# Optimization experiments

Measured on AMD Instinct MI355X. Metric: run time of the kernel, lower is better.

## Reference

```python
import jax, jax.numpy as jnp
import numpy as np

B, T, F, H = 16, 1024, 1024, 16
D = F // H  # 64

def setup_inputs() -> dict:
    key = jax.random.key(0)
    k0, k1, k2 = jax.random.split(key, 3)
    return {
        "x": jax.random.normal(k0, (B, T, F), jnp.float32),
        "mask": jnp.zeros((B, 1, T, 1), jnp.float32),
        "W_attn": jax.random.normal(k1, (F, 3 * F), jnp.float32) * 0.02,
        "b_attn": jnp.zeros((3 * F,), jnp.float32),
        "W_proj": jax.random.normal(k2, (F, F), jnp.float32) * 0.02,
        "b_proj": jnp.zeros((F,), jnp.float32),
    }

def reference(x, mask, W_attn, b_attn, W_proj, b_proj):
    # qkv projection (Conv1D == linear with transposed weight layout)
    qkv = x @ W_attn + b_attn                       # [B,T,3F]
    q, k, v = jnp.split(qkv, 3, axis=-1)
    split = lambda t: t.reshape(B, T, H, D).transpose(0, 2, 1, 3)  # [B,H,T,D]
    q, k, v = split(q), split(k), split(v)
    # non-standard: contract over T -> [B,H,D,D] score matrix
    s = jnp.einsum('bhtd,bhte->bhde', q, k) / jnp.sqrt(jnp.float32(D))
    tril = jnp.tril(jnp.ones((D, D), bool))         # bias buffer sliced to DxD
    s = jnp.where(tril, s, jnp.float32(-10000.0))
    # second matmul with V (before softmax), scaled by dk^2
    w = jnp.einsum('bhde,bhte->bhtd', s, v) / (jnp.float32(D) ** 2)  # [B,H,T,D]
    w = jax.nn.softmax(w + mask, axis=-2)           # softmax over T (dim=-2)
    a = w * v                                        # elementwise, not weighted sum
    merge = lambda t: t.transpose(0, 2, 1, 3).reshape(B, T, F)
    a = merge(a) @ W_proj + b_proj                   # output projection
    return a, merge(w)
```

## Files before the change

### kernel.cpp

```cpp
#include <hip/hip_runtime.h>
#include <math.h>

namespace {
constexpr int B = 16, T = 1024, F = 1024, H = 16, D = 64;
constexpr int NT = B * T;
constexpr int QKV_COLS = 3 * F;

constexpr size_t XHI_OFF = 0;
constexpr size_t XLO_OFF = 33554432;
constexpr size_t WAH_OFF = 67108864;
constexpr size_t WVL_OFF = 73400320;
constexpr size_t QB_OFF  = 75497472;
constexpr size_t KB_OFF  = 109051904;
constexpr size_t SB_OFF  = 142606336;
constexpr size_t AB_OFF  = 146800640;
constexpr size_t WPB_OFF = 180355072;
constexpr size_t VB_OFF   = QB_OFF;
constexpr size_t WRAW_OFF = XHI_OFF;
constexpr size_t SP_OFF   = WVL_OFF;
}

typedef __attribute__((ext_vector_type(8))) __bf16 bf16x8;
typedef __attribute__((ext_vector_type(4))) float f32x4;

__device__ __forceinline__ unsigned short f2bf(float f) {
  unsigned u = __builtin_bit_cast(unsigned, f);
  u += 0x7FFFu + ((u >> 16) & 1u);
  return (unsigned short)(u >> 16);
}
__device__ __forceinline__ float bf2f(unsigned short s) {
  return __builtin_bit_cast(float, (unsigned)s << 16);
}
__device__ __forceinline__ void gld16(const unsigned short* g, unsigned short* l) {
  __builtin_amdgcn_global_load_lds(
      (const __attribute__((address_space(1))) unsigned int*)g,
      (__attribute__((address_space(3))) unsigned int*)l, 16, 0, 0);
}

__global__ __launch_bounds__(256) void cast_x(const float* __restrict__ x,
                                              unsigned short* __restrict__ xhi,
                                              unsigned short* __restrict__ xlo) {
  int i = (blockIdx.x * 256 + threadIdx.x) * 4;
  float4 v = *(const float4*)&x[i];
  ushort4 h, l;
  h.x = f2bf(v.x); l.x = f2bf(v.x - bf2f(h.x));
  h.y = f2bf(v.y); l.y = f2bf(v.y - bf2f(h.y));
  h.z = f2bf(v.z); l.z = f2bf(v.z - bf2f(h.z));
  h.w = f2bf(v.w); l.w = f2bf(v.w - bf2f(h.w));
  *(ushort4*)&xhi[i] = h;
  *(ushort4*)&xlo[i] = l;
}

__global__ __launch_bounds__(256) void tcast(const float* __restrict__ W,
                                             unsigned short* __restrict__ Wt,
                                             unsigned short* __restrict__ Wlo,
                                             int ncols, int locol0) {
  __shared__ float tile[64][65];
  const int bx = blockIdx.x, by = blockIdx.y, tid = threadIdx.x;
#pragma unroll
  for (int i = 0; i < 16; ++i) {
    int idx = tid + i * 256;
    int r = idx >> 6, c = idx & 63;
    tile[r][c] = W[(size_t)(by * 64 + r) * ncols + bx * 64 + c];
  }
  __syncthreads();
#pragma unroll
  for (int i = 0; i < 16; ++i) {
    int idx = tid + i * 256;
    int r = idx >> 6, c = idx & 63;
    int col = bx * 64 + r;
    float w = tile[c][r];
    unsigned short h = f2bf(w);
    Wt[(size_t)col * 1024 + by * 64 + c] = h;
    if (col >= locol0) {
      Wlo[(size_t)(col - locol0) * 1024 + by * 64 + c] = f2bf(w - bf2f(h));
    }
  }
}

__device__ __forceinline__ void stage256(const unsigned short* __restrict__ Ag,
                                         const unsigned short* __restrict__ Bg,
                                         int row0, int col0, int kin,
                                         unsigned short* lbase, int wave,
                                         int lane) {
  const int rsub = lane >> 3;
  const int logb = ((lane & 7) ^ rsub) << 4;
  const int isB = logb >> 6;
  const int koff = kin + ((logb & 63) >> 1);
#pragma unroll
  for (int L = 0; L < 4; ++L) {
    const int R0 = (L * 8 + wave) * 8;
    const int r = R0 + rsub;
    const unsigned short* src =
        isB ? (Bg + (size_t)(col0 + r) * 1024 + koff)
            : (Ag + (size_t)(row0 + r) * 1024 + koff);
    gld16(src, lbase + (size_t)R0 * 64);
  }
}

template <int MODE>
__global__ __launch_bounds__(512, 2) void gemm256(
    const unsigned short* __restrict__ A0, const unsigned short* __restrict__ A1,
    const unsigned short* __restrict__ B0, const unsigned short* __restrict__ B1,
    const float* __restrict__ bias, void* __restrict__ out0,
    void* __restrict__ out1) {
  __shared__ __align__(16) unsigned short lds[2][256][64];
  const int tid = threadIdx.x;
  const int wave = tid >> 6, lane = tid & 63;
  const int wr = wave >> 2, wc = wave & 3;
  const int m16 = lane & 15, quad = lane >> 4;
  const int row0 = blockIdx.y * 256, col0 = blockIdx.x * 256;
  constexpr int NKT = (MODE == 1) ? 96 : 32;
  f32x4 acc[8][4] = {};

  stage256(A0, B0, row0, col0, 0, &lds[0][0][0], wave, lane);

  int cur = 0;
  for (int kt = 0; kt < NKT; ++kt) {
    if (kt + 1 < NKT) {
      const unsigned short* Ag = A0;
      const unsigned short* Bg = B0;
      int kin;
      if constexpr (MODE == 1) {
        const int kn = kt + 1, seg = kn >> 5;
        kin = (kn & 31) << 5;
        if (seg == 1) Ag = A1;
        if (seg == 2) Bg = B1;
      } else {
        kin = (kt + 1) << 5;
      }
      stage256(Ag, Bg, row0, col0, kin, &lds[cur ^ 1][0][0], wave, lane);
      asm volatile("s_waitcnt vmcnt(4)" ::: "memory");
    } else {
      asm volatile("s_waitcnt vmcnt(0)" ::: "memory");
    }
    __builtin_amdgcn_s_barrier();

    const char* tb = (const char*)&lds[cur][0][0];
#pragma unroll
    for (int ph = 0; ph < 2; ++ph) {
      bf16x8 af[4], bfr[4];
#pragma unroll
      for (int i = 0; i < 4; ++i) {
        const int r = wr * 128 + (ph * 4 + i) * 16 + m16;
        af[i] = *(const bf16x8*)(tb + r * 128 +
                                 ((quad * 16) ^ ((r & 7) << 4)));
      }
#pragma unroll
      for (int j = 0; j < 4; ++j) {
        const int c = wc * 64 + j * 16 + m16;
        bfr[j] = *(const bf16x8*)(tb + c * 128 +
                                  ((64 + quad * 16) ^ ((c & 7) << 4)));
      }
      __builtin_amdgcn_s_barrier();
      asm volatile("s_waitcnt lgkmcnt(0)" ::: "memory");
      __builtin_amdgcn_sched_barrier(0);
      __builtin_amdgcn_s_setprio(1);
#pragma unroll
      for (int i = 0; i < 4; ++i)
#pragma unroll
        for (int j = 0; j < 4; ++j)
          acc[ph * 4 + i][j] = __builtin_amdgcn_mfma_f32_16x16x32_bf16(
              af[i], bfr[j], acc[ph * 4 + i][j], 0, 0, 0);
      __builtin_amdgcn_s_setprio(0);
      __builtin_amdgcn_s_barrier();
    }
    cur ^= 1;
  }

  if constexpr (MODE == 0) {
    unsigned short* dst = (col0 >= 1024) ? (unsigned short*)out1
                                         : (unsigned short*)out0;
#pragma unroll
    for (int j = 0; j < 4; ++j) {
      const int gcol = col0 + wc * 64 + j * 16 + m16;
      const int f = gcol & 1023;
      const int h = f >> 6, dd = f & 63;
      const float bv = bias[gcol];
#pragma unroll
      for (int i = 0; i < 8; ++i) {
#pragma unroll
        for (int r = 0; r < 4; ++r) {
          const int grow = row0 + wr * 128 + i * 16 + quad * 4 + r;
          const int b = grow >> 10, t = grow & 1023;
          dst[(((size_t)b * H + h) * T + t) * D + dd] = f2bf(acc[i][j][r] + bv);
        }
      }
    }
  } else if constexpr (MODE == 1) {
    float* vbp = (float*)out0;
#pragma unroll
    for (int j = 0; j < 4; ++j) {
      const int f = col0 + wc * 64 + j * 16 + m16;
      const int h = f >> 6, dd = f & 63;
      const float bv = bias[f];
#pragma unroll
      for (int i = 0; i < 8; ++i) {
#pragma unroll
        for (int r = 0; r < 4; ++r) {
          const int grow = row0 + wr * 128 + i * 16 + quad * 4 + r;
          const int b = grow >> 10, t = grow & 1023;
          vbp[(((size_t)b * H + h) * T + t) * D + dd] = acc[i][j][r] + bv;
        }
      }
    }
  } else {
    float* o = (float*)out0;
#pragma unroll
    for (int j = 0; j < 4; ++j) {
      const int gcol = col0 + wc * 64 + j * 16 + m16;
      const float bv = bias[gcol];
#pragma unroll
      for (int i = 0; i < 8; ++i) {
#pragma unroll
        for (int r = 0; r < 4; ++r) {
          const int grow = row0 + wr * 128 + i * 16 + quad * 4 + r;
          o[(size_t)grow * F + gcol] = acc[i][j][r] + bv;
        }
      }
    }
  }
}

__global__ __launch_bounds__(256) void score_kernel(
    const unsigned short* __restrict__ qb, const unsigned short* __restrict__ kb,
    float* __restrict__ sb) {
  __shared__ float qs[64][65];
  __shared__ float ks[64][65];
  const int bh = blockIdx.x;
  const int tid = threadIdx.x;
  const size_t base = (size_t)bh * T * D;
  const int d0 = (tid >> 4) * 4, e0 = (tid & 15) * 4;
  float acc[4][4] = {};
  for (int ch = 0; ch < T / 64; ++ch) {
#pragma unroll
    for (int i = 0; i < 4; ++i) {
      int idx = (tid + i * 256) * 4;
      ushort4 qv = *(const ushort4*)&qb[base + (size_t)ch * 4096 + idx];
      ushort4 kv = *(const ushort4*)&kb[base + (size_t)ch * 4096 + idx];
      int r = idx >> 6, c = idx & 63;
      qs[r][c] = bf2f(qv.x); qs[r][c+1] = bf2f(qv.y);
      qs[r][c+2] = bf2f(qv.z); qs[r][c+3] = bf2f(qv.w);
      ks[r][c] = bf2f(kv.x); ks[r][c+1] = bf2f(kv.y);
      ks[r][c+2] = bf2f(kv.z); ks[r][c+3] = bf2f(kv.w);
    }
    __syncthreads();
#pragma unroll 8
    for (int tt = 0; tt < 64; ++tt) {
      float qa[4], kv[4];
#pragma unroll
      for (int i = 0; i < 4; ++i) qa[i] = qs[tt][d0 + i];
#pragma unroll
      for (int j = 0; j < 4; ++j) kv[j] = ks[tt][e0 + j];
#pragma unroll
      for (int i = 0; i < 4; ++i)
#pragma unroll
        for (int j = 0; j < 4; ++j) acc[i][j] += qa[i] * kv[j];
    }
    __syncthreads();
  }
#pragma unroll
  for (int i = 0; i < 4; ++i) {
#pragma unroll
    for (int j = 0; j < 4; ++j) {
      int dd = d0 + i, ee = e0 + j;
      float v = acc[i][j] * 0.125f;
      if (ee > dd) v = -10000.0f;
      sb[(size_t)bh * (D * D) + dd * D + ee] = v;
    }
  }
}

__global__ __launch_bounds__(256) void exp_kernel(
    const float* __restrict__ vb, const float* __restrict__ sb,
    const float* __restrict__ mask, float* __restrict__ wraw,
    float* __restrict__ sp) {
  const int tc = blockIdx.x, bh = blockIdx.y;
  const int b = bh >> 4;
  const int tid = threadIdx.x;
  const int lane = tid & 63;
  const int dg = __builtin_amdgcn_readfirstlane(tid >> 6);
  const int tg = tc * 64 + lane;
  const float* vrow = vb + (size_t)bh * (T * D) + (size_t)tg * D;
  float4 vreg[16];
#pragma unroll
  for (int i = 0; i < 16; ++i) vreg[i] = *(const float4*)&vrow[i * 4];
  const float mval = mask[(size_t)b * T + tg];
  float ex[16];
#pragma unroll
  for (int dd = 0; dd < 16; ++dd) {
    const int d = dg * 16 + dd;
    const float* srow = sb + (size_t)bh * 4096 + (size_t)d * 64;
    float acc = 0.f;
#pragma unroll
    for (int e4 = 0; e4 < 16; ++e4) {
      float4 s4 = *(const float4*)&srow[e4 * 4];
      acc += s4.x * vreg[e4].x + s4.y * vreg[e4].y +
             s4.z * vreg[e4].z + s4.w * vreg[e4].w;
    }
    float w = acc * (1.0f / 4096.0f) + mval;
    ex[dd] = __expf(w);
    wraw[(size_t)bh * (T * D) + (size_t)d * T + tg] = ex[dd];
  }
#pragma unroll
  for (int dd = 0; dd < 16; ++dd) {
    float v = ex[dd];
    v += __shfl_xor(v, 1, 64);
    v += __shfl_xor(v, 2, 64);
    v += __shfl_xor(v, 4, 64);
    v += __shfl_xor(v, 8, 64);
    v += __shfl_xor(v, 16, 64);
    v += __shfl_xor(v, 32, 64);
    if (lane == 0) sp[((size_t)bh * 16 + tc) * 64 + dg * 16 + dd] = v;
  }
}

__global__ __launch_bounds__(256) void norm_kernel(
    const float* __restrict__ vb, const float* __restrict__ wraw,
    const float* __restrict__ sp, unsigned short* __restrict__ ab,
    float* __restrict__ out2) {
  __shared__ float wt[64][65];
  __shared__ float invS[64];
  const int tc = blockIdx.x, bh = blockIdx.y;
  const int b = bh >> 4, h = bh & 15;
  const int tid = threadIdx.x;
  if (tid < 64) {
    float S = 0.f;
#pragma unroll
    for (int j = 0; j < 16; ++j) S += sp[((size_t)bh * 16 + j) * 64 + tid];
    invS[tid] = 1.0f / S;
  }
#pragma unroll
  for (int i = 0; i < 16; ++i) {
    int idx = tid + i * 256;
    int dd = idx >> 6, tt = idx & 63;
    wt[dd][tt] = wraw[(size_t)bh * (T * D) + (size_t)dd * T + tc * 64 + tt];
  }
  __syncthreads();
  const int d = tid & 63, trow = tid >> 6;
#pragma unroll
  for (int j = 0; j < 16; ++j) {
    int tl = trow * 16 + j;
    int tg = tc * 64 + tl;
    float o = wt[d][tl] * invS[d];
    float vv = vb[(size_t)bh * (T * D) + (size_t)tg * D + d];
    size_t oidx = ((size_t)b * T + tg) * F + h * 64 + d;
    out2[oidx] = o;
    ab[oidx] = f2bf(o * vv);
  }
}

extern "C" void kernel_launch(void* const* d_in, const int* in_sizes, int n_in,
                              void* d_out, int out_size, void* d_ws,
                              size_t ws_size, hipStream_t stream) {
  const float* x = (const float*)d_in[0];
  const float* mask = (const float*)d_in[1];
  const float* Wa = (const float*)d_in[2];
  const float* ba = (const float*)d_in[3];
  const float* Wp = (const float*)d_in[4];
  const float* bp = (const float*)d_in[5];
  char* ws = (char*)d_ws;
  float* out = (float*)d_out;

  unsigned short* xhi = (unsigned short*)(ws + XHI_OFF);
  unsigned short* xlo = (unsigned short*)(ws + XLO_OFF);
  unsigned short* Wah = (unsigned short*)(ws + WAH_OFF);
  unsigned short* Wvl = (unsigned short*)(ws + WVL_OFF);
  unsigned short* qb  = (unsigned short*)(ws + QB_OFF);
  unsigned short* kb  = (unsigned short*)(ws + KB_OFF);
  float* sb   = (float*)(ws + SB_OFF);
  unsigned short* ab  = (unsigned short*)(ws + AB_OFF);
  unsigned short* Wpb = (unsigned short*)(ws + WPB_OFF);
  float* vb   = (float*)(ws + VB_OFF);
  float* wraw = (float*)(ws + WRAW_OFF);
  float* sp   = (float*)(ws + SP_OFF);

  cast_x<<<NT * F / 1024, 256, 0, stream>>>(x, xhi, xlo);
  tcast<<<dim3(QKV_COLS / 64, F / 64), 256, 0, stream>>>(Wa, Wah, Wvl,
                                                         QKV_COLS, 2048);
  tcast<<<dim3(F / 64, F / 64), 256, 0, stream>>>(Wp, Wpb, Wvl, F, 1 << 30);

  gemm256<0><<<dim3(2048 / 256, NT / 256), 512, 0, stream>>>(
      xhi, nullptr, Wah, nullptr, ba, qb, kb);

  score_kernel<<<dim3(B * H), 256, 0, stream>>>(qb, kb, sb);

  gemm256<1><<<dim3(F / 256, NT / 256), 512, 0, stream>>>(
      xhi, xlo, Wah + (size_t)2048 * 1024, Wvl, ba + 2048, vb, nullptr);

  exp_kernel<<<dim3(T / 64, B * H), 256, 0, stream>>>(vb, sb, mask, wraw, sp);

  norm_kernel<<<dim3(T / 64, B * H), 256, 0, stream>>>(
      vb, wraw, sp, ab, out + (size_t)NT * F);

  gemm256<2><<<dim3(F / 256, NT / 256), 512, 0, stream>>>(
      ab, nullptr, Wpb, nullptr, bp, out, nullptr);
}
```

Baseline: 638.4 us.

## Deepen GEMM LDS pipeline to four buffers with three tiles in flight

New measurement: 630.3 us. Within noise of the previous version (-1.3%).

```diff
diff --git a/kernel.cpp b/kernel.cpp
--- a/kernel.cpp
+++ b/kernel.cpp
@@ -99,12 +99,29 @@
 }
 
 template <int MODE>
+__device__ __forceinline__ void tile_src(
+    int kt, const unsigned short* __restrict__ A0,
+    const unsigned short* __restrict__ A1,
+    const unsigned short* __restrict__ B0,
+    const unsigned short* __restrict__ B1,
+    const unsigned short*& Ag, const unsigned short*& Bg, int& kin) {
+  if constexpr (MODE == 1) {
+    const int seg = kt >> 5;
+    kin = (kt & 31) << 5;
+    Ag = (seg == 1) ? A1 : A0;
+    Bg = (seg == 2) ? B1 : B0;
+  } else {
+    Ag = A0; Bg = B0; kin = kt << 5;
+  }
+}
+
+template <int MODE>
 __global__ __launch_bounds__(512, 2) void gemm256(
     const unsigned short* __restrict__ A0, const unsigned short* __restrict__ A1,
     const unsigned short* __restrict__ B0, const unsigned short* __restrict__ B1,
     const float* __restrict__ bias, void* __restrict__ out0,
     void* __restrict__ out1) {
-  __shared__ __align__(16) unsigned short lds[2][256][64];
+  __shared__ __align__(16) unsigned short lds[4][256][64];
   const int tid = threadIdx.x;
   const int wave = tid >> 6, lane = tid & 63;
   const int wr = wave >> 2, wc = wave & 3;
@@ -113,59 +130,64 @@
   constexpr int NKT = (MODE == 1) ? 96 : 32;
   f32x4 acc[8][4] = {};
 
-  stage256(A0, B0, row0, col0, 0, &lds[0][0][0], wave, lane);
-
-  int cur = 0;
+#pragma unroll
+  for (int p = 0; p < 3; ++p) {
+    const unsigned short *Ag, *Bg; int kin;
+    tile_src<MODE>(p, A0, A1, B0, B1, Ag, Bg, kin);
+    stage256(Ag, Bg, row0, col0, kin, &lds[p][0][0], wave, lane);
+  }
+
   for (int kt = 0; kt < NKT; ++kt) {
-    if (kt + 1 < NKT) {
-      const unsigned short* Ag = A0;
-      const unsigned short* Bg = B0;
-      int kin;
-      if constexpr (MODE == 1) {
-        const int kn = kt + 1, seg = kn >> 5;
-        kin = (kn & 31) << 5;
-        if (seg == 1) Ag = A1;
-        if (seg == 2) Bg = B1;
-      } else {
-        kin = (kt + 1) << 5;
-      }
-      stage256(Ag, Bg, row0, col0, kin, &lds[cur ^ 1][0][0], wave, lane);
-      asm volatile("s_waitcnt vmcnt(4)" ::: "memory");
+    if (kt + 3 < NKT) {
+      const unsigned short *Ag, *Bg; int kin;
+      tile_src<MODE>(kt + 3, A0, A1, B0, B1, Ag, Bg, kin);
+      stage256(Ag, Bg, row0, col0, kin, &lds[(kt + 3) & 3][0][0], wave, lane);
+      asm volatile("s_waitcnt vmcnt(12)" ::: "memory");
     } else {
-      asm volatile("s_waitcnt vmcnt(0)" ::: "memory");
+      const int rem = NKT - 1 - kt;
+      if (rem == 2)      asm volatile("s_waitcnt vmcnt(8)" ::: "memory");
+      else if (rem == 1) asm volatile("s_waitcnt vmcnt(4)" ::: "memory");
+      else               asm volatile("s_waitcnt vmcnt(0)" ::: "memory");
     }
     __builtin_amdgcn_s_barrier();
-
-    const char* tb = (const char*)&lds[cur][0][0];
-#pragma unroll
-    for (int ph = 0; ph < 2; ++ph) {
-      bf16x8 af[4], bfr[4];
-#pragma unroll
-      for (int i = 0; i < 4; ++i) {
-        const int r = wr * 128 + (ph * 4 + i) * 16 + m16;
-        af[i] = *(const bf16x8*)(tb + r * 128 +
-                                 ((quad * 16) ^ ((r & 7) << 4)));
-      }
-#pragma unroll
-      for (int j = 0; j < 4; ++j) {
-        const int c = wc * 64 + j * 16 + m16;
-        bfr[j] = *(const bf16x8*)(tb + c * 128 +
-                                  ((64 + quad * 16) ^ ((c & 7) << 4)));
-      }
-      __builtin_amdgcn_s_barrier();
-      asm volatile("s_waitcnt lgkmcnt(0)" ::: "memory");
-      __builtin_amdgcn_sched_barrier(0);
-      __builtin_amdgcn_s_setprio(1);
-#pragma unroll
-      for (int i = 0; i < 4; ++i)
-#pragma unroll
-        for (int j = 0; j < 4; ++j)
-          acc[ph * 4 + i][j] = __builtin_amdgcn_mfma_f32_16x16x32_bf16(
-              af[i], bfr[j], acc[ph * 4 + i][j], 0, 0, 0);
-      __builtin_amdgcn_s_setprio(0);
-      __builtin_amdgcn_s_barrier();
-    }
-    cur ^= 1;
+    __builtin_amdgcn_sched_barrier(0);
+
+    const char* tb = (const char*)&lds[kt & 3][0][0];
+    bf16x8 bfr[4], af0[4], af1[4];
+#pragma unroll
+    for (int j = 0; j < 4; ++j) {
+      const int c = wc * 64 + j * 16 + m16;
+      bfr[j] = *(const bf16x8*)(tb + c * 128 +
+                                ((64 + quad * 16) ^ ((c & 7) << 4)));
+    }
+#pragma unroll
+    for (int i = 0; i < 4; ++i) {
+      const int r = wr * 128 + i * 16 + m16;
+      af0[i] = *(const bf16x8*)(tb + r * 128 +
+                                ((quad * 16) ^ ((r & 7) << 4)));
+    }
+#pragma unroll
+    for (int i = 0; i < 4; ++i) {
+      const int r = wr * 128 + 64 + i * 16 + m16;
+      af1[i] = *(const bf16x8*)(tb + r * 128 +
+                                ((quad * 16) ^ ((r & 7) << 4)));
+    }
+    __builtin_amdgcn_s_setprio(1);
+#pragma unroll
+    for (int i = 0; i < 4; ++i)
+#pragma unroll
+      for (int j = 0; j < 4; ++j)
+        acc[i][j] = __builtin_amdgcn_mfma_f32_16x16x32_bf16(
+            af0[i], bfr[j], acc[i][j], 0, 0, 0);
+#pragma unroll
+    for (int i = 0; i < 4; ++i)
+#pragma unroll
+      for (int j = 0; j < 4; ++j)
+        acc[4 + i][j] = __builtin_amdgcn_mfma_f32_16x16x32_bf16(
+            af1[i], bfr[j], acc[4 + i][j], 0, 0, 0);
+    __builtin_amdgcn_s_setprio(0);
+    __builtin_amdgcn_s_barrier();
+    __builtin_amdgcn_sched_barrier(0);
   }
 
   if constexpr (MODE == 0) {
```
